# Kernel optimization log

Measured on AMD Instinct MI355X. Metric: run time of the kernel, lower is better.

Reference implementation:

```python
import jax, jax.numpy as jnp
import numpy as np

INPUT_DIM = 16
BLOCK_LEVELS = 17
OUT_DIM = 5  # dim_weight


def setup_inputs() -> dict:
    key = jax.random.key(0)
    ks = jax.random.split(key, 17)
    B, H, HS = 4096, 1024, 3
    s = 0.05  # keep activations bounded through stacked relu-linears
    return {
        "x": jax.random.normal(ks[0], (B, INPUT_DIM), jnp.float32),
        "Win_f": jax.random.normal(ks[1], (BLOCK_LEVELS, 96, H), jnp.float32) * s,
        "bin_f": jax.random.normal(ks[2], (BLOCK_LEVELS, H), jnp.float32) * s,
        "Win_b": jax.random.normal(ks[3], (BLOCK_LEVELS, 96, H), jnp.float32) * s,
        "bin_b": jax.random.normal(ks[4], (BLOCK_LEVELS, H), jnp.float32) * s,
        "Wblk": jax.random.normal(ks[5], (HS, H, H), jnp.float32) * (s / 2),
        "bblk": jax.random.normal(ks[6], (HS, H), jnp.float32) * s,
        "Wout_f": jax.random.normal(ks[7], (BLOCK_LEVELS, H, OUT_DIM), jnp.float32) * s,
        "bout_f": jax.random.normal(ks[8], (BLOCK_LEVELS, OUT_DIM), jnp.float32) * s,
        "Wout_b": jax.random.normal(ks[9], (BLOCK_LEVELS, H, OUT_DIM), jnp.float32) * s,
        "bout_b": jax.random.normal(ks[10], (BLOCK_LEVELS, OUT_DIM), jnp.float32) * s,
        "W1": jax.random.normal(ks[11], (OUT_DIM, OUT_DIM), jnp.float32) * s,
        "W2": jax.random.normal(ks[12], (OUT_DIM, OUT_DIM), jnp.float32) * s,
        "W3": jax.random.normal(ks[13], (OUT_DIM, OUT_DIM), jnp.float32) * s,
        "W4": jax.random.normal(ks[14], (OUT_DIM * BLOCK_LEVELS, OUT_DIM * BLOCK_LEVELS), jnp.float32) * s,
        "b4": jax.random.normal(ks[15], (OUT_DIM * BLOCK_LEVELS,), jnp.float32) * s,
    }


def _run_direction(x, Win, bin_, Wblk, bblk, Wout, bout):
    # Sequential growing-concat stack: level i takes [x, out_0..out_{i-1}]
    # (width 16 + 5*i). Block weights Wblk are SHARED across all levels.
    outs = []
    prev = x
    for i in range(BLOCK_LEVELS):
        w = Win[i, : INPUT_DIM + OUT_DIM * i, :]  # static slice of padded weight
        h = prev @ w + bin_[i]
        for j in range(Wblk.shape[0]):  # Dropout(p=0) -> Linear -> ReLU
            h = jax.nn.relu(h @ Wblk[j] + bblk[j])
        out = h @ Wout[i] + bout[i]  # (B, 5)
        outs.append(out)
        prev = jnp.concatenate([x] + outs, axis=1)
    return jnp.concatenate(outs, axis=1)  # (B, 85)


def reference(x, Win_f, bin_f, Win_b, bin_b, Wblk, bblk,
              Wout_f, bout_f, Wout_b, bout_b, W1, W2, W3, W4, b4):
    B = x.shape[0]
    tot_f = _run_direction(x, Win_f, bin_f, Wblk, bblk, Wout_f, bout_f)
    tot_b = _run_direction(x, Win_b, bin_b, Wblk, bblk, Wout_b, bout_b)
    tf = tot_f.reshape(B, OUT_DIM, BLOCK_LEVELS)            # (B, 5, 17)
    tb = tot_b.reshape(B, OUT_DIM, BLOCK_LEVELS)[:, :, ::-1]  # reversed levels
    # small attention: q=(B,17,5), k=(B,5,17), v=(B,17,5)
    q = jnp.einsum('bdt,de->bte', tf, W1)
    k = jnp.einsum('bdt,de->bet', tb, W2)
    v = jnp.einsum('bdt,de->bte', tb, W3)
    scores = jnp.einsum('bte,bes->bts', q, k)  # (B, 17, 17)
    attn = jax.nn.softmax(scores, axis=1)      # NB: softmax over dim=1, as in source
    res = jnp.einsum('bts,bse->bte', attn, v)  # (B, 17, 5)
    return res.reshape(B, -1) @ W4 + b4        # (B, 85)
```

## Files before the change

### kernel.cpp

```cpp
#include <hip/hip_runtime.h>
#include <hip/hip_fp16.h>

#define H 1024
#define NLEV 17
#define OD 5
#define TOTD 85
#define PW 128
#define NB 4096

typedef _Float16 half8 __attribute__((ext_vector_type(8)));
typedef float f32x4 __attribute__((ext_vector_type(4)));

__device__ __forceinline__ void g2l16(const void* g, void* l) {
  __builtin_amdgcn_global_load_lds((const __attribute__((address_space(1))) unsigned*)g,
                                   (__attribute__((address_space(3))) unsigned*)l, 16, 0, 0);
}

template<int KSTEPS, bool RELU>
__global__ __launch_bounds__(256, 2)
void gemm_k(const _Float16* __restrict__ A, int ldaB,
            const _Float16* __restrict__ B0, const _Float16* __restrict__ B1, int ldbB,
            const float* __restrict__ bias0, const float* __restrict__ bias1,
            _Float16* __restrict__ C) {
  __shared__ _Float16 sA[128 * 64];
  __shared__ _Float16 sB[128 * 64];
  const int tid = threadIdx.x;
  const int lane = tid & 63;
  const int wave = tid >> 6;
  const int wm = wave >> 1, wn = wave & 1;
  const int mt = blockIdx.x, nt = blockIdx.y;
  const _Float16* Bp = (mt < 32) ? B0 : B1;
  const float* bias = (mt < 32) ? bias0 : bias1;

  char* sAc = (char*)sA;
  char* sBc = (char*)sB;

  const int srow = (lane >> 3);
  const int scb = (lane & 7) << 4;

  f32x4 acc[4][4];
#pragma unroll
  for (int m = 0; m < 4; ++m)
#pragma unroll
    for (int n = 0; n < 4; ++n) acc[m][n] = 0.f;

  const char* Ab = (const char*)A + (size_t)(mt * 128) * ldaB;
  const char* Bb = (const char*)Bp + (size_t)(nt * 128) * ldbB;

  for (int ks = 0; ks < KSTEPS; ++ks) {
    const int kB = ks << 7;
#pragma unroll
    for (int t = 0; t < 4; ++t) {
      int chunk = wave * 4 + t;
      int row = chunk * 8 + srow;
      int off = kB + (scb ^ ((row & 7) << 4));
      g2l16(Ab + (size_t)row * ldaB + off, sAc + chunk * 1024);
      g2l16(Bb + (size_t)row * ldbB + off, sBc + chunk * 1024);
    }
    __syncthreads();
#pragma unroll
    for (int h = 0; h < 2; ++h) {
      half8 af[4], bf[4];
      int kb = h * 64 + ((lane >> 4) << 4);
#pragma unroll
      for (int m = 0; m < 4; ++m) {
        int row = wm * 64 + m * 16 + (lane & 15);
        af[m] = *(const half8*)(sAc + row * 128 + (kb ^ ((row & 7) << 4)));
      }
#pragma unroll
      for (int n = 0; n < 4; ++n) {
        int row = wn * 64 + n * 16 + (lane & 15);
        bf[n] = *(const half8*)(sBc + row * 128 + (kb ^ ((row & 7) << 4)));
      }
#pragma unroll
      for (int m = 0; m < 4; ++m)
#pragma unroll
        for (int n = 0; n < 4; ++n)
          acc[m][n] = __builtin_amdgcn_mfma_f32_16x16x32_f16(af[m], bf[n], acc[m][n], 0, 0, 0);
    }
    __syncthreads();
  }
  const int r0 = mt * 128 + wm * 64 + (lane >> 4) * 4;
#pragma unroll
  for (int n = 0; n < 4; ++n) {
    int col = nt * 128 + wn * 64 + n * 16 + (lane & 15);
    float bv = bias[col];
#pragma unroll
    for (int m = 0; m < 4; ++m) {
      int rbase = r0 + m * 16;
#pragma unroll
      for (int r = 0; r < 4; ++r) {
        float v = acc[m][n][r] + bv;
        if (RELU) v = v > 0.f ? v : 0.f;
        C[(size_t)(rbase + r) * H + col] = (_Float16)v;
      }
    }
  }
}

__global__ __launch_bounds__(256)
void outproj_k(const _Float16* __restrict__ h3,
               const float* __restrict__ Wout_f, const float* __restrict__ Wout_b,
               const float* __restrict__ bout_f, const float* __restrict__ bout_b,
               int lev, float* __restrict__ tot, _Float16* __restrict__ P) {
  int gw = blockIdx.x * 4 + (threadIdx.x >> 6);
  int lane = threadIdx.x & 63;
  int dir = gw >> 12;
  int b = gw & 4095;
  const _Float16* hr = h3 + (size_t)gw * H;
  const float* Wo = (dir ? Wout_b : Wout_f) + (size_t)lev * H * OD;
  const float* bo = (dir ? bout_b : bout_f) + lev * OD;
  float acc[OD] = {0.f, 0.f, 0.f, 0.f, 0.f};
  for (int j = 0; j < 16; ++j) {
    int k = j * 64 + lane;
    float hv = (float)hr[k];
#pragma unroll
    for (int d = 0; d < OD; ++d) acc[d] += hv * Wo[k * OD + d];
  }
#pragma unroll
  for (int off = 32; off; off >>= 1)
#pragma unroll
    for (int d = 0; d < OD; ++d) acc[d] += __shfl_xor(acc[d], off);
  if (lane == 0) {
#pragma unroll
    for (int d = 0; d < OD; ++d) {
      float v = acc[d] + bo[d];
      tot[(size_t)dir * NB * TOTD + (size_t)b * TOTD + lev * OD + d] = v;
      P[((size_t)(dir * NB + b)) * PW + 16 + OD * lev + d] = (_Float16)v;
    }
  }
}

__global__ __launch_bounds__(128)
void attn_k(const float* __restrict__ tot, const float* __restrict__ W1,
            const float* __restrict__ W2, const float* __restrict__ W3,
            const float* __restrict__ W4, const float* __restrict__ b4,
            float* __restrict__ out) {
  __shared__ float tf[5][17], tbr[5][17];
  __shared__ float q[17][5], k2[5][17], vv[17][5];
  __shared__ float sc[17][17];
  __shared__ float res[85];
  int b = blockIdx.x, tid = threadIdx.x;
  const float* tfp = tot + (size_t)b * TOTD;
  const float* tbp = tot + (size_t)NB * TOTD + (size_t)b * TOTD;
  if (tid < 85) {
    int c = tid / 17, t = tid % 17;
    tf[c][t] = tfp[tid];
    tbr[c][t] = tbp[c * 17 + (16 - t)];
  }
  __syncthreads();
  if (tid < 85) {
    int t = tid / 5, e = tid % 5;
    float qa = 0, ka = 0, va = 0;
#pragma unroll
    for (int c = 0; c < 5; ++c) {
      qa += tf[c][t] * W1[c * 5 + e];
      ka += tbr[c][t] * W2[c * 5 + e];
      va += tbr[c][t] * W3[c * 5 + e];
    }
    q[t][e] = qa; k2[e][t] = ka; vv[t][e] = va;
  }
  __syncthreads();
  for (int idx = tid; idx < 289; idx += 128) {
    int t = idx / 17, s = idx % 17;
    float a = 0;
#pragma unroll
    for (int e = 0; e < 5; ++e) a += q[t][e] * k2[e][s];
    sc[t][s] = a;
  }
  __syncthreads();
  if (tid < 17) {
    int s = tid;
    float m = -1e30f;
#pragma unroll
    for (int t = 0; t < 17; ++t) m = fmaxf(m, sc[t][s]);
    float ex[17];
    float sum = 0;
#pragma unroll
    for (int t = 0; t < 17; ++t) { ex[t] = expf(sc[t][s] - m); sum += ex[t]; }
    float inv = 1.f / sum;
#pragma unroll
    for (int t = 0; t < 17; ++t) sc[t][s] = ex[t] * inv;
  }
  __syncthreads();
  if (tid < 85) {
    int t = tid / 5, e = tid % 5;
    float a = 0;
#pragma unroll
    for (int s = 0; s < 17; ++s) a += sc[t][s] * vv[s][e];
    res[tid] = a;
  }
  __syncthreads();
  if (tid < 85) {
    float a = b4[tid];
    for (int s = 0; s < 85; ++s) a += res[s] * W4[s * 85 + tid];
    out[(size_t)b * TOTD + tid] = a;
  }
}

__global__ __launch_bounds__(256)
void prep_wblk(const float* __restrict__ Wblk, _Float16* __restrict__ WblkT) {
  int idx = blockIdx.x * 256 + threadIdx.x;
  int j = idx >> 20;
  int rem = idx & 1048575;
  int n = rem >> 10, k = rem & 1023;
  WblkT[idx] = (_Float16)Wblk[((size_t)j << 20) + ((size_t)k << 10) + n];
}

__global__ __launch_bounds__(256)
void prep_win(const float* __restrict__ Wf, const float* __restrict__ Wb,
              _Float16* __restrict__ WT) {
  int idx = blockIdx.x * 256 + threadIdx.x;
  int d = idx / (17 * 1024 * 128);
  int rem = idx % (17 * 1024 * 128);
  int i = rem / (1024 * 128);
  int r2 = rem % (1024 * 128);
  int n = r2 >> 7, k = r2 & 127;
  const float* W = d ? Wb : Wf;
  WT[idx] = (k < 96) ? (_Float16)W[((size_t)i * 96 + k) * 1024 + n] : (_Float16)0.f;
}

__global__ __launch_bounds__(256)
void prep_p(const float* __restrict__ x, _Float16* __restrict__ P) {
  int idx = blockIdx.x * 256 + threadIdx.x;
  int r = idx >> 7, c = idx & 127;
  int b = r & 4095;
  P[idx] = (c < 16) ? (_Float16)x[b * 16 + c] : (_Float16)0.f;
}

extern "C" void kernel_launch(void* const* d_in, const int* in_sizes, int n_in,
                              void* d_out, int out_size, void* d_ws, size_t ws_size,
                              hipStream_t stream) {
  const float* x = (const float*)d_in[0];
  const float* Win_f = (const float*)d_in[1];
  const float* bin_f = (const float*)d_in[2];
  const float* Win_b = (const float*)d_in[3];
  const float* bin_b = (const float*)d_in[4];
  const float* Wblk = (const float*)d_in[5];
  const float* bblk = (const float*)d_in[6];
  const float* Wout_f = (const float*)d_in[7];
  const float* bout_f = (const float*)d_in[8];
  const float* Wout_b = (const float*)d_in[9];
  const float* bout_b = (const float*)d_in[10];
  const float* W1 = (const float*)d_in[11];
  const float* W2 = (const float*)d_in[12];
  const float* W3 = (const float*)d_in[13];
  const float* W4 = (const float*)d_in[14];
  const float* b4 = (const float*)d_in[15];
  float* out = (float*)d_out;

  char* ws = (char*)d_ws;
  size_t off = 0;
  auto alloc = [&](size_t bytes) {
    void* p = ws + off;
    off += (bytes + 255) & ~(size_t)255;
    return p;
  };
  _Float16* WblkT = (_Float16*)alloc((size_t)3 * 1024 * 1024 * 2);
  _Float16* WinT = (_Float16*)alloc((size_t)2 * 17 * 1024 * 128 * 2);
  _Float16* P = (_Float16*)alloc((size_t)8192 * 128 * 2);
  _Float16* hA = (_Float16*)alloc((size_t)8192 * 1024 * 2);
  _Float16* hB = (_Float16*)alloc((size_t)8192 * 1024 * 2);
  float* tot = (float*)alloc((size_t)2 * NB * TOTD * 4);

  prep_wblk<<<dim3(3 * 1024 * 1024 / 256), dim3(256), 0, stream>>>(Wblk, WblkT);
  prep_win<<<dim3(2 * 17 * 1024 * 128 / 256), dim3(256), 0, stream>>>(Win_f, Win_b, WinT);
  prep_p<<<dim3(8192 * 128 / 256), dim3(256), 0, stream>>>(x, P);

  dim3 ggrid(64, 8), gblk(256);
  for (int i = 0; i < NLEV; ++i) {
    gemm_k<2, false><<<ggrid, gblk, 0, stream>>>(
        P, PW * 2, WinT + (size_t)i * 1024 * 128, WinT + (size_t)(NLEV + i) * 1024 * 128,
        PW * 2, bin_f + i * H, bin_b + i * H, hA);
    gemm_k<16, true><<<ggrid, gblk, 0, stream>>>(
        hA, H * 2, WblkT, WblkT, H * 2, bblk, bblk, hB);
    gemm_k<16, true><<<ggrid, gblk, 0, stream>>>(
        hB, H * 2, WblkT + (1 << 20), WblkT + (1 << 20), H * 2, bblk + H, bblk + H, hA);
    gemm_k<16, true><<<ggrid, gblk, 0, stream>>>(
        hA, H * 2, WblkT + (2 << 20), WblkT + (2 << 20), H * 2, bblk + 2 * H, bblk + 2 * H, hB);
    outproj_k<<<dim3(2048), dim3(256), 0, stream>>>(
        hB, Wout_f, Wout_b, bout_f, bout_b, i, tot, P);
  }
  attn_k<<<dim3(NB), dim3(128), 0, stream>>>(tot, W1, W2, W3, W4, b4, out);
}
```

Baseline: 1.556 ms.

## Fuse output projection into last block GEMM and trim input GEMM K

The third block GEMM now reduces its ReLU tile against Wout in registers and atomically adds per-row partial sums into tot, which removes the separate outproj kernel and the final 8192x1024 h write and read. The input-projection GEMM becomes a new kernel that reads x and prior level outputs directly from fp16 x and fp32 tot, and runs only as many K-steps as the current concat width needs instead of a fixed 128. Weight transpose prep kernels use shared-memory tiles so global accesses are coalesced. The cost is atomics on tot (which needs zeroing first, so summation order is nondeterministic) and an LDS-free input GEMM with scattered loads.

```diff
diff --git a/kernel.cpp b/kernel.cpp
--- a/kernel.cpp
+++ b/kernel.cpp
@@ -5,7 +5,6 @@
 #define NLEV 17
 #define OD 5
 #define TOTD 85
-#define PW 128
 #define NB 4096
 
 typedef _Float16 half8 __attribute__((ext_vector_type(8)));
@@ -16,12 +15,15 @@
                                    (__attribute__((address_space(3))) unsigned*)l, 16, 0, 0);
 }
 
-template<int KSTEPS, bool RELU>
+template<int NT, bool RELU, bool FUSE>
 __global__ __launch_bounds__(256, 2)
 void gemm_k(const _Float16* __restrict__ A, int ldaB,
             const _Float16* __restrict__ B0, const _Float16* __restrict__ B1, int ldbB,
             const float* __restrict__ bias0, const float* __restrict__ bias1,
-            _Float16* __restrict__ C) {
+            _Float16* __restrict__ C,
+            const float* __restrict__ Wout_f, const float* __restrict__ Wout_b,
+            const float* __restrict__ bout_f, const float* __restrict__ bout_b,
+            int lev, float* __restrict__ tot) {
   __shared__ _Float16 sA[128 * 64];
   __shared__ _Float16 sB[128 * 64];
   const int tid = threadIdx.x;
@@ -47,7 +49,7 @@
   const char* Ab = (const char*)A + (size_t)(mt * 128) * ldaB;
   const char* Bb = (const char*)Bp + (size_t)(nt * 128) * ldbB;
 
-  for (int ks = 0; ks < KSTEPS; ++ks) {
+  for (int ks = 0; ks < NT; ++ks) {
     const int kB = ks << 7;
 #pragma unroll
     for (int t = 0; t < 4; ++t) {
@@ -80,54 +82,129 @@
     }
     __syncthreads();
   }
-  const int r0 = mt * 128 + wm * 64 + (lane >> 4) * 4;
+
+  const int r0 = mt * 128 + wm * 64 + ((lane >> 4) << 2);
+  int cols[4];
+  float bv[4];
 #pragma unroll
   for (int n = 0; n < 4; ++n) {
-    int col = nt * 128 + wn * 64 + n * 16 + (lane & 15);
-    float bv = bias[col];
+    cols[n] = nt * 128 + wn * 64 + n * 16 + (lane & 15);
+    bv[n] = bias[cols[n]];
+  }
+  float wo[4][OD];
+  const float* boB = nullptr;
+  if constexpr (FUSE) {
+    const float* WoB = ((mt >= 32) ? Wout_b : Wout_f) + (size_t)lev * H * OD;
+#pragma unroll
+    for (int n = 0; n < 4; ++n)
+#pragma unroll
+      for (int d = 0; d < OD; ++d) wo[n][d] = WoB[cols[n] * OD + d];
+    boB = ((mt >= 32) ? bout_b : bout_f) + lev * OD;
+  }
+#pragma unroll
+  for (int m = 0; m < 4; ++m) {
+#pragma unroll
+    for (int r = 0; r < 4; ++r) {
+      float p[OD] = {0.f, 0.f, 0.f, 0.f, 0.f};
+#pragma unroll
+      for (int n = 0; n < 4; ++n) {
+        float v = acc[m][n][r] + bv[n];
+        if (RELU) v = fmaxf(v, 0.f);
+        if constexpr (!FUSE) {
+          C[(size_t)(r0 + m * 16 + r) * H + cols[n]] = (_Float16)v;
+        } else {
+#pragma unroll
+          for (int d = 0; d < OD; ++d) p[d] += v * wo[n][d];
+        }
+      }
+      if constexpr (FUSE) {
+#pragma unroll
+        for (int d = 0; d < OD; ++d) {
+          p[d] += __shfl_xor(p[d], 1);
+          p[d] += __shfl_xor(p[d], 2);
+          p[d] += __shfl_xor(p[d], 4);
+          p[d] += __shfl_xor(p[d], 8);
+        }
+        if ((lane & 15) == 0) {
+          int row = r0 + m * 16 + r;
+          int bb = row & 4095;
+          int dir = row >> 12;
+          float* tp = tot + (size_t)dir * NB * TOTD + (size_t)bb * TOTD + lev * OD;
+#pragma unroll
+          for (int d = 0; d < OD; ++d) {
+            float add = p[d];
+            if (nt == 0 && wn == 0) add += boB[d];
+            atomicAdd(tp + d, add);
+          }
+        }
+      }
+    }
+  }
+}
+
+__global__ __launch_bounds__(256)
+void gemmin_k(const _Float16* __restrict__ x16, const float* __restrict__ tot,
+              const _Float16* __restrict__ WinT,
+              const float* __restrict__ bin_f, const float* __restrict__ bin_b,
+              int lev, int nsteps, _Float16* __restrict__ Cout) {
+  const int tid = threadIdx.x;
+  const int lane = tid & 63;
+  const int wave = tid >> 6;
+  const int wm = wave >> 1, wn = wave & 1;
+  const int mt = blockIdx.x;
+  const int nt = blockIdx.y;
+  const int dir = mt >> 5;
+  const float* bias = dir ? bin_b : bin_f;
+  const _Float16* Wl = WinT + ((size_t)(dir * NLEV + lev) << 17);
+  const int cl = lane & 15;
+  const int kg = lane >> 4;
+  const int rbase = mt * 128 + wm * 64;
+
+  f32x4 acc[4][4];
+#pragma unroll
+  for (int m = 0; m < 4; ++m)
+#pragma unroll
+    for (int n = 0; n < 4; ++n) acc[m][n] = 0.f;
+
+#pragma unroll 1
+  for (int s = 0; s < nsteps; ++s) {
+    const int kc = s * 32 + kg * 8;
+    half8 aF[4], bF[4];
 #pragma unroll
     for (int m = 0; m < 4; ++m) {
-      int rbase = r0 + m * 16;
-#pragma unroll
-      for (int r = 0; r < 4; ++r) {
-        float v = acc[m][n][r] + bv;
-        if (RELU) v = v > 0.f ? v : 0.f;
-        C[(size_t)(rbase + r) * H + col] = (_Float16)v;
-      }
-    }
-  }
-}
-
-__global__ __launch_bounds__(256)
-void outproj_k(const _Float16* __restrict__ h3,
-               const float* __restrict__ Wout_f, const float* __restrict__ Wout_b,
-               const float* __restrict__ bout_f, const float* __restrict__ bout_b,
-               int lev, float* __restrict__ tot, _Float16* __restrict__ P) {
-  int gw = blockIdx.x * 4 + (threadIdx.x >> 6);
-  int lane = threadIdx.x & 63;
-  int dir = gw >> 12;
-  int b = gw & 4095;
-  const _Float16* hr = h3 + (size_t)gw * H;
-  const float* Wo = (dir ? Wout_b : Wout_f) + (size_t)lev * H * OD;
-  const float* bo = (dir ? bout_b : bout_f) + lev * OD;
-  float acc[OD] = {0.f, 0.f, 0.f, 0.f, 0.f};
-  for (int j = 0; j < 16; ++j) {
-    int k = j * 64 + lane;
-    float hv = (float)hr[k];
-#pragma unroll
-    for (int d = 0; d < OD; ++d) acc[d] += hv * Wo[k * OD + d];
-  }
-#pragma unroll
-  for (int off = 32; off; off >>= 1)
-#pragma unroll
-    for (int d = 0; d < OD; ++d) acc[d] += __shfl_xor(acc[d], off);
-  if (lane == 0) {
-#pragma unroll
-    for (int d = 0; d < OD; ++d) {
-      float v = acc[d] + bo[d];
-      tot[(size_t)dir * NB * TOTD + (size_t)b * TOTD + lev * OD + d] = v;
-      P[((size_t)(dir * NB + b)) * PW + 16 + OD * lev + d] = (_Float16)v;
-    }
+      int b = (rbase + m * 16 + cl) & 4095;
+      if (kc < 16) {
+        aF[m] = *(const half8*)(x16 + b * 16 + kc);
+      } else {
+        const float* tp = tot + (size_t)dir * NB * TOTD + (size_t)b * TOTD + (kc - 16);
+        half8 h;
+#pragma unroll
+        for (int e = 0; e < 8; ++e) h[e] = (_Float16)tp[e];
+        aF[m] = h;
+      }
+    }
+#pragma unroll
+    for (int n = 0; n < 4; ++n) {
+      int col = nt * 128 + wn * 64 + n * 16 + cl;
+      bF[n] = *(const half8*)(Wl + (size_t)col * 128 + kc);
+    }
+#pragma unroll
+    for (int m = 0; m < 4; ++m)
+#pragma unroll
+      for (int n = 0; n < 4; ++n)
+        acc[m][n] = __builtin_amdgcn_mfma_f32_16x16x32_f16(aF[m], bF[n], acc[m][n], 0, 0, 0);
+  }
+
+  const int r0 = mt * 128 + wm * 64 + (kg << 2);
+#pragma unroll
+  for (int n = 0; n < 4; ++n) {
+    int col = nt * 128 + wn * 64 + n * 16 + cl;
+    float bvn = bias[col];
+#pragma unroll
+    for (int m = 0; m < 4; ++m)
+#pragma unroll
+      for (int r = 0; r < 4; ++r)
+        Cout[(size_t)(r0 + m * 16 + r) * H + col] = (_Float16)(acc[m][n][r] + bvn);
   }
 }
 
@@ -199,42 +276,67 @@
 }
 
 __global__ __launch_bounds__(256)
-void prep_wblk(const float* __restrict__ Wblk, _Float16* __restrict__ WblkT) {
+void prep_wblkT(const float* __restrict__ W, _Float16* __restrict__ WT) {
+  __shared__ float tile[32][33];
+  const int j = blockIdx.z;
+  const int n0 = blockIdx.x * 32, k0 = blockIdx.y * 32;
+  const int c = threadIdx.x & 31, r8 = threadIdx.x >> 5;
+  const float* Wj = W + ((size_t)j << 20);
+  _Float16* WTj = WT + ((size_t)j << 20);
+#pragma unroll
+  for (int i = 0; i < 4; ++i) {
+    int r = r8 + i * 8;
+    tile[r][c] = Wj[(size_t)(k0 + r) * 1024 + n0 + c];
+  }
+  __syncthreads();
+#pragma unroll
+  for (int i = 0; i < 4; ++i) {
+    int r = r8 + i * 8;
+    WTj[(size_t)(n0 + r) * 1024 + k0 + c] = (_Float16)tile[c][r];
+  }
+}
+
+__global__ __launch_bounds__(256)
+void prep_winT(const float* __restrict__ Wf, const float* __restrict__ Wb,
+               _Float16* __restrict__ WT) {
+  __shared__ float tile[32][33];
+  const int z = blockIdx.z;
+  const int d = z / NLEV, lev = z % NLEV;
+  const int n0 = blockIdx.x * 32, k0 = blockIdx.y * 32;
+  const float* W = (d ? Wb : Wf) + (size_t)lev * 96 * 1024;
+  _Float16* WTl = WT + ((size_t)(d * NLEV + lev) << 17);
+  const int c = threadIdx.x & 31, r8 = threadIdx.x >> 5;
+#pragma unroll
+  for (int i = 0; i < 4; ++i) {
+    int r = r8 + i * 8;
+    int k = k0 + r;
+    tile[r][c] = (k < 96) ? W[(size_t)k * 1024 + n0 + c] : 0.f;
+  }
+  __syncthreads();
+#pragma unroll
+  for (int i = 0; i < 4; ++i) {
+    int r = r8 + i * 8;
+    WTl[(size_t)(n0 + r) * 128 + k0 + c] = (_Float16)tile[c][r];
+  }
+}
+
+__global__ __launch_bounds__(256)
+void prep_x16(const float* __restrict__ x, _Float16* __restrict__ x16) {
   int idx = blockIdx.x * 256 + threadIdx.x;
-  int j = idx >> 20;
-  int rem = idx & 1048575;
-  int n = rem >> 10, k = rem & 1023;
-  WblkT[idx] = (_Float16)Wblk[((size_t)j << 20) + ((size_t)k << 10) + n];
-}
-
-__global__ __launch_bounds__(256)
-void prep_win(const float* __restrict__ Wf, const float* __restrict__ Wb,
-              _Float16* __restrict__ WT) {
+  x16[idx] = (_Float16)x[idx];
+}
+
+__global__ __launch_bounds__(256)
+void zero_tot(float* __restrict__ tot) {
   int idx = blockIdx.x * 256 + threadIdx.x;
-  int d = idx / (17 * 1024 * 128);
-  int rem = idx % (17 * 1024 * 128);
-  int i = rem / (1024 * 128);
-  int r2 = rem % (1024 * 128);
-  int n = r2 >> 7, k = r2 & 127;
-  const float* W = d ? Wb : Wf;
-  WT[idx] = (k < 96) ? (_Float16)W[((size_t)i * 96 + k) * 1024 + n] : (_Float16)0.f;
-}
-
-__global__ __launch_bounds__(256)
-void prep_p(const float* __restrict__ x, _Float16* __restrict__ P) {
-  int idx = blockIdx.x * 256 + threadIdx.x;
-  int r = idx >> 7, c = idx & 127;
-  int b = r & 4095;
-  P[idx] = (c < 16) ? (_Float16)x[b * 16 + c] : (_Float16)0.f;
+  tot[idx] = 0.f;
 }
 
 extern "C" void kernel_launch(void* const* d_in, const int* in_sizes, int n_in,
                               void* d_out, int out_size, void* d_ws, size_t ws_size,
                               hipStream_t stream) {
   const float* x = (const float*)d_in[0];
-  const float* Win_f = (const float*)d_in[1];
   const float* bin_f = (const float*)d_in[2];
-  const float* Win_b = (const float*)d_in[3];
   const float* bin_b = (const float*)d_in[4];
   const float* Wblk = (const float*)d_in[5];
   const float* bblk = (const float*)d_in[6];
@@ -257,29 +359,31 @@
     return p;
   };
   _Float16* WblkT = (_Float16*)alloc((size_t)3 * 1024 * 1024 * 2);
-  _Float16* WinT = (_Float16*)alloc((size_t)2 * 17 * 1024 * 128 * 2);
-  _Float16* P = (_Float16*)alloc((size_t)8192 * 128 * 2);
+  _Float16* WinT = (_Float16*)alloc((size_t)2 * NLEV * 1024 * 128 * 2);
+  _Float16* x16 = (_Float16*)alloc((size_t)4096 * 16 * 2);
   _Float16* hA = (_Float16*)alloc((size_t)8192 * 1024 * 2);
   _Float16* hB = (_Float16*)alloc((size_t)8192 * 1024 * 2);
   float* tot = (float*)alloc((size_t)2 * NB * TOTD * 4);
 
-  prep_wblk<<<dim3(3 * 1024 * 1024 / 256), dim3(256), 0, stream>>>(Wblk, WblkT);
-  prep_win<<<dim3(2 * 17 * 1024 * 128 / 256), dim3(256), 0, stream>>>(Win_f, Win_b, WinT);
-  prep_p<<<dim3(8192 * 128 / 256), dim3(256), 0, stream>>>(x, P);
+  prep_wblkT<<<dim3(32, 32, 3), dim3(256), 0, stream>>>(Wblk, WblkT);
+  prep_winT<<<dim3(32, 4, 2 * NLEV), dim3(256), 0, stream>>>(
+      (const float*)d_in[1], (const float*)d_in[3], WinT);
+  prep_x16<<<dim3(256), dim3(256), 0, stream>>>(x, x16);
+  zero_tot<<<dim3(2720), dim3(256), 0, stream>>>(tot);
 
   dim3 ggrid(64, 8), gblk(256);
   for (int i = 0; i < NLEV; ++i) {
-    gemm_k<2, false><<<ggrid, gblk, 0, stream>>>(
-        P, PW * 2, WinT + (size_t)i * 1024 * 128, WinT + (size_t)(NLEV + i) * 1024 * 128,
-        PW * 2, bin_f + i * H, bin_b + i * H, hA);
-    gemm_k<16, true><<<ggrid, gblk, 0, stream>>>(
-        hA, H * 2, WblkT, WblkT, H * 2, bblk, bblk, hB);
-    gemm_k<16, true><<<ggrid, gblk, 0, stream>>>(
-        hB, H * 2, WblkT + (1 << 20), WblkT + (1 << 20), H * 2, bblk + H, bblk + H, hA);
-    gemm_k<16, true><<<ggrid, gblk, 0, stream>>>(
-        hA, H * 2, WblkT + (2 << 20), WblkT + (2 << 20), H * 2, bblk + 2 * H, bblk + 2 * H, hB);
-    outproj_k<<<dim3(2048), dim3(256), 0, stream>>>(
-        hB, Wout_f, Wout_b, bout_f, bout_b, i, tot, P);
+    int nsteps = (16 + 5 * i + 31) / 32;
+    gemmin_k<<<ggrid, gblk, 0, stream>>>(x16, tot, WinT, bin_f, bin_b, i, nsteps, hA);
+    gemm_k<16, true, false><<<ggrid, gblk, 0, stream>>>(
+        hA, H * 2, WblkT, WblkT, H * 2, bblk, bblk, hB,
+        nullptr, nullptr, nullptr, nullptr, 0, nullptr);
+    gemm_k<16, true, false><<<ggrid, gblk, 0, stream>>>(
+        hB, H * 2, WblkT + (1 << 20), WblkT + (1 << 20), H * 2, bblk + H, bblk + H, hA,
+        nullptr, nullptr, nullptr, nullptr, 0, nullptr);
+    gemm_k<16, true, true><<<ggrid, gblk, 0, stream>>>(
+        hA, H * 2, WblkT + (2 << 20), WblkT + (2 << 20), H * 2, bblk + 2 * H, bblk + 2 * H, hB,
+        Wout_f, Wout_b, bout_f, bout_b, i, tot);
   }
   attn_k<<<dim3(NB), dim3(128), 0, stream>>>(tot, W1, W2, W3, W4, b4, out);
 }
```

After: 1.931 ms. 1.24x slower.
